# Performance work log

Hardware: AMD Instinct MI355X
Metric: run time of the kernel (lower is better)

## Reference

```python
import jax, jax.numpy as jnp
from jax import lax
import numpy as np

ALIGN = 6                 # AlignW: pad width up to a multiple of align_width=6
W_BITS = 5
A_BITS = 5
A_MASK = (1 << A_BITS) - 1  # direct_conv2d bit-packs activations: keep low A_bits
DN = ('NCHW', 'OIHW', 'NCHW')


def _align_w(a):
    pad = (-a.shape[-1]) % ALIGN
    if pad:
        a = jnp.pad(a, ((0, 0), (0, 0), (0, 0), (0, pad)))
    return a


def _conv_relu(a, w, b):
    # nn.Conv2d(kernel_size=3, padding=2) + ReLU
    y = lax.conv_general_dilated(a, w, (1, 1), [(2, 2), (2, 2)], dimension_numbers=DN)
    return jax.nn.relu(y + b[None, :, None, None])


def _dc_conv(a, w):
    # DC_layer: integer direct conv2d, W_bits-quantized weights, A_bits activations,
    # stride 1, no padding (valid).
    aq = jnp.bitwise_and(a, A_MASK)
    return lax.conv_general_dilated(aq, w, (1, 1), [(0, 0), (0, 0)], dimension_numbers=DN,
                                    preferred_element_type=jnp.int32)


def _maxpool2(a):
    if jnp.issubdtype(a.dtype, jnp.floating):
        init = np.float32(-np.inf)
    else:
        init = np.int32(np.iinfo(np.int32).min)
    return lax.reduce_window(a, init, lax.max, (1, 1, 2, 2), (1, 1, 2, 2), 'VALID')


def _forward(x, ws, bs, qs, fc_w, fc_b):
    a = x
    k = 0
    for n in (2, 2, 3):          # float VGG blocks: [64,64,M, 128,128,M, 256,256,256,M]
        for _ in range(n):
            a = _conv_relu(_align_w(a), ws[k], bs[k])
            k += 1
        a = _maxpool2(a)
    # dequant stub is identity; x.int() truncates toward zero (a >= 0 after ReLU)
    xi = lax.stop_gradient(a).astype(jnp.int32)
    k = 0
    for n in (3, 3):             # DC blocks: [512,512,512,M, 512,512,512,M]
        for _ in range(n):
            xi = _dc_conv(_align_w(xi), qs[k])
            k += 1
        xi = _maxpool2(xi)
    # classifier: AdaptiveAvgPool2d((1,1)) + Flatten + Linear(512, 1000)
    pooled = jnp.mean(xi.astype(jnp.float32), axis=(2, 3))
    return pooled @ fc_w.T + fc_b


def setup_inputs() -> dict:
    key = jax.random.key(0)
    ks = jax.random.split(key, 24)
    d = {}
    d['x'] = jax.random.uniform(ks[0], (16, 3, 224, 224), jnp.float32) * 8.0
    conv_cfg = [(3, 64), (64, 64), (64, 128), (128, 128), (128, 256), (256, 256), (256, 256)]
    for i, (ci, co) in enumerate(conv_cfg):
        d[f'w{i + 1}'] = jax.random.normal(ks[1 + i], (co, ci, 3, 3), jnp.float32) * 0.1
        d[f'b{i + 1}'] = jax.random.normal(ks[8 + i], (co,), jnp.float32) * 0.1
    dc_cfg = [(256, 512)] + [(512, 512)] * 5
    for i, (ci, co) in enumerate(dc_cfg):
        # torch.randint(0, 2**W_bits - 1, ...) -> values in [0, 2**W_bits - 2]
        d[f'q{i + 1}'] = jax.random.randint(ks[15 + i], (co, ci, 3, 3), 0, 2 ** W_BITS - 1, jnp.int32)
    d['fc_w'] = jax.random.normal(ks[21], (1000, 512), jnp.float32) * 0.02
    d['fc_b'] = jnp.zeros((1000,), jnp.float32)
    return d


def reference(x, w1, w2, w3, w4, w5, w6, w7,
              b1, b2, b3, b4, b5, b6, b7,
              q1, q2, q3, q4, q5, q6, fc_w, fc_b):
    ws = (w1, w2, w3, w4, w5, w6, w7)
    bs = (b1, b2, b3, b4, b5, b6, b7)
    qs = (q1, q2, q3, q4, q5, q6)
    return _forward(x, ws, bs, qs, fc_w, fc_b)
```

## Files before the change

### kernel.cpp

```cpp
#include <hip/hip_runtime.h>
#include <cstddef>


typedef float v2f __attribute__((ext_vector_type(2)));

static __device__ __forceinline__ int dot4(int a, int b, int c) {
#if __has_builtin(__builtin_amdgcn_sdot4)
    return __builtin_amdgcn_sdot4(a, b, c, false);
#else
    return c + (a & 255) * (b & 255)
             + ((a >> 8) & 255) * ((b >> 8) & 255)
             + ((a >> 16) & 255) * ((b >> 16) & 255)
             + ((a >> 24) & 255) * ((b >> 24) & 255);
#endif
}

static __device__ __forceinline__ void ld6f(const float* __restrict__ p, float v[6]) {
    const float4 a = *reinterpret_cast<const float4*>(p);
    const float2 b = *reinterpret_cast<const float2*>(p + 4);
    v[0] = a.x; v[1] = a.y; v[2] = a.z; v[3] = a.w; v[4] = b.x; v[5] = b.y;
}
static __device__ __forceinline__ void ld6i(const int* __restrict__ p, int v[6]) {
    const int4 a = *reinterpret_cast<const int4*>(p);
    const int2 b = *reinterpret_cast<const int2*>(p + 4);
    v[0] = a.x; v[1] = a.y; v[2] = a.z; v[3] = a.w; v[4] = b.x; v[5] = b.y;
}

static __device__ __forceinline__ void fmac8(const float v[3][6],
                                             const float* __restrict__ wr,
                                             v2f acc[8][2])
{
#pragma unroll
    for (int kh = 0; kh < 3; ++kh) {
        const v2f P0 = {v[kh][0], v[kh][1]};
        const v2f P1 = {v[kh][1], v[kh][2]};
        const v2f P2 = {v[kh][2], v[kh][3]};
        const v2f Q1 = {v[kh][3], v[kh][4]};
        const v2f Q2 = {v[kh][4], v[kh][5]};
#pragma unroll
        for (int c = 0; c < 8; ++c) {
            const float k0 = wr[c * 9 + kh * 3 + 0];
            const float k1 = wr[c * 9 + kh * 3 + 1];
            const float k2 = wr[c * 9 + kh * 3 + 2];
            const v2f k0p = {k0, k0}, k1p = {k1, k1}, k2p = {k2, k2};
            v2f a0 = acc[c][0];
            a0 = __builtin_elementwise_fma(P2, k2p, a0);
            a0 = __builtin_elementwise_fma(P1, k1p, a0);
            a0 = __builtin_elementwise_fma(P0, k0p, a0);
            acc[c][0] = a0;
            v2f a1 = acc[c][1];
            a1 = __builtin_elementwise_fma(Q2, k2p, a1);
            a1 = __builtin_elementwise_fma(Q1, k1p, a1);
            a1 = __builtin_elementwise_fma(P2, k0p, a1);
            acc[c][1] = a1;
        }
    }
}

static __device__ __forceinline__ void fmac4p(const float v[4][6],
                                              const float* __restrict__ wr,
                                              v2f acc[4][2][2])
{
#pragma unroll
    for (int r = 0; r < 2; ++r) {
#pragma unroll
        for (int kh = 0; kh < 3; ++kh) {
            const float* vv = v[r + kh];
            const v2f P0 = {vv[0], vv[1]};
            const v2f P1 = {vv[1], vv[2]};
            const v2f P2 = {vv[2], vv[3]};
            const v2f Q1 = {vv[3], vv[4]};
            const v2f Q2 = {vv[4], vv[5]};
#pragma unroll
            for (int c = 0; c < 4; ++c) {
                const float k0 = wr[c * 9 + kh * 3 + 0];
                const float k1 = wr[c * 9 + kh * 3 + 1];
                const float k2 = wr[c * 9 + kh * 3 + 2];
                const v2f k0p = {k0, k0}, k1p = {k1, k1}, k2p = {k2, k2};
                v2f a0 = acc[c][r][0];
                a0 = __builtin_elementwise_fma(P2, k2p, a0);
                a0 = __builtin_elementwise_fma(P1, k1p, a0);
                a0 = __builtin_elementwise_fma(P0, k0p, a0);
                acc[c][r][0] = a0;
                v2f a1 = acc[c][r][1];
                a1 = __builtin_elementwise_fma(Q2, k2p, a1);
                a1 = __builtin_elementwise_fma(Q1, k1p, a1);
                a1 = __builtin_elementwise_fma(P2, k0p, a1);
                acc[c][r][1] = a1;
            }
        }
    }
}

static __device__ __forceinline__ void dotc8(const int v[3][6],
                                             const int* __restrict__ wr,
                                             int acc[8][4])
{
#pragma unroll
    for (int kh = 0; kh < 3; ++kh) {
#pragma unroll
        for (int c = 0; c < 8; ++c) {
            const int k0 = wr[c * 9 + kh * 3 + 0];
            const int k1 = wr[c * 9 + kh * 3 + 1];
            const int k2 = wr[c * 9 + kh * 3 + 2];
#pragma unroll
            for (int t = 0; t < 4; ++t)
                acc[c][t] = dot4(v[kh][t], k0,
                            dot4(v[kh][t + 1], k1,
                            dot4(v[kh][t + 2], k2, acc[c][t])));
        }
    }
}

template<int CIN,int PH,int PW,int OH,int OW,int OPW,bool BORDER>
__global__ __launch_bounds__(256) void convf_k(
    const float* __restrict__ in, int instr,
    const float* __restrict__ wfp, const float* __restrict__ bias,
    float* __restrict__ out, int outstr, int total)
{
    constexpr int WB  = (OW + 3) / 4;
    constexpr int OPH = BORDER ? OH + 4 : OH;
    constexpr int OPL = OPH * OPW;
    const int s = blockIdx.z * 256 + threadIdx.x;
    if (s >= total) return;
    const int wb = s % WB;
    const int h  = (s / WB) % OH;
    const int n  = s / (WB * OH);
    const int w0 = wb * 4;
    const int cob = blockIdx.x;
    const int co0 = cob * 8;

    const float* ip = in + (size_t)n * instr + (size_t)h * PW + w0;
    const float* wl = wfp + (size_t)cob * CIN * 72;

    v2f acc[8][2];
#pragma unroll
    for (int c = 0; c < 8; ++c) { acc[c][0] = (v2f)0.f; acc[c][1] = (v2f)0.f; }

    float vb[3][6], vn[3][6];
#pragma unroll
    for (int kh = 0; kh < 3; ++kh) ld6f(ip + kh * PW, vb[kh]);

    if constexpr ((CIN & 1) == 0) {
        for (int ci = 0; ci < CIN; ci += 2) {
            ip += PH * PW;
#pragma unroll
            for (int kh = 0; kh < 3; ++kh) ld6f(ip + kh * PW, vn[kh]);
            fmac8(vb, wl + (size_t)ci * 72, acc);
            ip += PH * PW;
#pragma unroll
            for (int kh = 0; kh < 3; ++kh) ld6f(ip + kh * PW, vb[kh]);
            fmac8(vn, wl + (size_t)(ci + 1) * 72, acc);
        }
    } else {
        for (int ci = 0; ci < CIN; ++ci) {
            ip += PH * PW;
#pragma unroll
            for (int kh = 0; kh < 3; ++kh) ld6f(ip + kh * PW, vn[kh]);
            fmac8(vb, wl + (size_t)ci * 72, acc);
#pragma unroll
            for (int kh = 0; kh < 3; ++kh)
#pragma unroll
                for (int j = 0; j < 6; ++j) vb[kh][j] = vn[kh][j];
        }
    }

    float* ob = out + (size_t)n * outstr;
    const int ph  = BORDER ? h + 2 : h;
    const int pwo = BORDER ? 2 : 0;
#pragma unroll
    for (int c = 0; c < 8; ++c) {
        float* plane = ob + (size_t)(co0 + c) * OPL;
        float* row = plane + (size_t)ph * OPW;
        const float b = bias[co0 + c];
        float av[4] = {acc[c][0][0], acc[c][0][1], acc[c][1][0], acc[c][1][1]};
#pragma unroll
        for (int t = 0; t < 4; ++t)
            if (w0 + t < OW) { const float r = av[t] + b; row[pwo + w0 + t] = r > 0.f ? r : 0.f; }
        if (BORDER) {
            if (wb == 0) { row[0] = 0.f; row[1] = 0.f; }
            if (wb == WB - 1) { for (int pw = OW + 2; pw < OPW; ++pw) row[pw] = 0.f; }
            if (h == 0 || h == OH - 1) {
                float* r0 = plane + (h == 0 ? 0 : (size_t)(OH + 2) * OPW);
                for (int rr = 0; rr < 2; ++rr) {
                    float* br = r0 + (size_t)rr * OPW;
#pragma unroll
                    for (int t = 0; t < 4; ++t) if (w0 + t < OW) br[2 + w0 + t] = 0.f;
                    if (wb == 0) { br[0] = 0.f; br[1] = 0.f; }
                    if (wb == WB - 1) { for (int pw = OW + 2; pw < OPW; ++pw) br[pw] = 0.f; }
                }
            }
        }
    }
}

template<int CIN,int PH,int PW,int POH,int POW,int OPW,int OY,int OX,bool TOINT>
__global__ __launch_bounds__(256) void convfp_k(
    const float* __restrict__ in, int instr,
    const float* __restrict__ wfp, const float* __restrict__ bias,
    void* __restrict__ outv, int outstr, int total)
{
    constexpr int WBp = POW / 2;
    constexpr int OPH = POH + 2 * OY;
    constexpr int OPL = OPH * OPW;
    const int s = blockIdx.z * 256 + threadIdx.x;
    if (s >= total) return;
    const int pb = s % WBp;
    const int ph = (s / WBp) % POH;
    const int n  = s / (WBp * POH);
    const int cob = blockIdx.x;
    const int co0 = cob * 4;

    const float* ip = in + (size_t)n * instr + (size_t)(2 * ph) * PW + 4 * pb;
    const float* wl = wfp + (size_t)cob * CIN * 36;

    v2f acc[4][2][2];
#pragma unroll
    for (int c = 0; c < 4; ++c)
#pragma unroll
        for (int r = 0; r < 2; ++r) { acc[c][r][0] = (v2f)0.f; acc[c][r][1] = (v2f)0.f; }

    float vb[4][6], vn[4][6];
#pragma unroll
    for (int r = 0; r < 4; ++r) ld6f(ip + r * PW, vb[r]);

    for (int ci = 0; ci < CIN; ci += 2) {
        ip += PH * PW;
#pragma unroll
        for (int r = 0; r < 4; ++r) ld6f(ip + r * PW, vn[r]);
        fmac4p(vb, wl + (size_t)ci * 36, acc);
        ip += PH * PW;
#pragma unroll
        for (int r = 0; r < 4; ++r) ld6f(ip + r * PW, vb[r]);
        fmac4p(vn, wl + (size_t)(ci + 1) * 36, acc);
    }

#pragma unroll
    for (int c = 0; c < 4; ++c) {
        const float b = bias[co0 + c];
        float r00 = acc[c][0][0][0] + b; r00 = r00 > 0.f ? r00 : 0.f;
        float r01 = acc[c][0][0][1] + b; r01 = r01 > 0.f ? r01 : 0.f;
        float r02 = acc[c][0][1][0] + b; r02 = r02 > 0.f ? r02 : 0.f;
        float r03 = acc[c][0][1][1] + b; r03 = r03 > 0.f ? r03 : 0.f;
        float r10 = acc[c][1][0][0] + b; r10 = r10 > 0.f ? r10 : 0.f;
        float r11 = acc[c][1][0][1] + b; r11 = r11 > 0.f ? r11 : 0.f;
        float r12 = acc[c][1][1][0] + b; r12 = r12 > 0.f ? r12 : 0.f;
        float r13 = acc[c][1][1][1] + b; r13 = r13 > 0.f ? r13 : 0.f;
        float p0 = r00; p0 = p0 > r01 ? p0 : r01; p0 = p0 > r10 ? p0 : r10; p0 = p0 > r11 ? p0 : r11;
        float p1 = r02; p1 = p1 > r03 ? p1 : r03; p1 = p1 > r12 ? p1 : r12; p1 = p1 > r13 ? p1 : r13;

        if constexpr (TOINT) {
            int* plane = (int*)outv + (size_t)n * outstr + (size_t)(co0 + c) * OPL;
            int* row = plane + (size_t)(OY + ph) * OPW;
            row[OX + 2 * pb]     = (int)p0;
            row[OX + 2 * pb + 1] = (int)p1;
            if (pb == WBp - 1) { for (int pw = OX + POW; pw < OPW; ++pw) row[pw] = 0; }
        } else {
            float* plane = (float*)outv + (size_t)n * outstr + (size_t)(co0 + c) * OPL;
            float* row = plane + (size_t)(OY + ph) * OPW;
            row[OX + 2 * pb]     = p0;
            row[OX + 2 * pb + 1] = p1;
            if (OX > 0 && pb == 0) { row[0] = 0.f; row[1] = 0.f; }
            if (pb == WBp - 1) { for (int pw = OX + POW; pw < OPW; ++pw) row[pw] = 0.f; }
            if (OY > 0 && (ph == 0 || ph == POH - 1)) {
                float* r0 = plane + (ph == 0 ? 0 : (size_t)(OY + POH) * OPW);
                for (int rr = 0; rr < OY; ++rr) {
                    float* br = r0 + (size_t)rr * OPW;
                    br[OX + 2 * pb] = 0.f; br[OX + 2 * pb + 1] = 0.f;
                    if (pb == 0) { br[0] = 0.f; br[1] = 0.f; }
                    if (pb == WBp - 1) { for (int pw = OX + POW; pw < OPW; ++pw) br[pw] = 0.f; }
                }
            }
        }
    }
}

template<int CIN4,int PH,int PW,int OH,int OW,int OPW,bool PACKOUT>
__global__ __launch_bounds__(256) void convq_k(
    const int* __restrict__ in, int instr, const int* __restrict__ wqp,
    int* __restrict__ out, int outstr, int total)
{
    constexpr int WB  = (OW + 3) / 4;
    constexpr int OPL = OH * OPW;
    const int s = blockIdx.z * 256 + threadIdx.x;
    if (s >= total) return;
    const int wb = s % WB;
    const int h  = (s / WB) % OH;
    const int n  = s / (WB * OH);
    const int w0 = wb * 4;
    const int cob = blockIdx.x;
    const int co0 = cob * 8;

    const int* ip = in + (size_t)n * instr + (size_t)h * PW + w0;
    const int* wl = wqp + (size_t)cob * CIN4 * 72;

    int acc[8][4];
#pragma unroll
    for (int c = 0; c < 8; ++c)
#pragma unroll
        for (int t = 0; t < 4; ++t) acc[c][t] = 0;

    int vb[3][6], vn[3][6];
#pragma unroll
    for (int kh = 0; kh < 3; ++kh) ld6i(ip + kh * PW, vb[kh]);

    for (int ci = 0; ci < CIN4; ci += 2) {
        ip += PH * PW;
#pragma unroll
        for (int kh = 0; kh < 3; ++kh) ld6i(ip + kh * PW, vn[kh]);
        dotc8(vb, wl + (size_t)ci * 72, acc);
        ip += PH * PW;
#pragma unroll
        for (int kh = 0; kh < 3; ++kh) ld6i(ip + kh * PW, vb[kh]);
        dotc8(vn, wl + (size_t)(ci + 1) * 72, acc);
    }

    if (PACKOUT) {
        int* base = out + (size_t)n * outstr + (size_t)(cob * 2) * OPL + (size_t)h * OPW + w0;
#pragma unroll
        for (int t = 0; t < 4; ++t) {
            if (w0 + t < OW) {
                const int lo = (acc[0][t] & 31) | ((acc[1][t] & 31) << 8)
                             | ((acc[2][t] & 31) << 16) | ((acc[3][t] & 31) << 24);
                const int hi = (acc[4][t] & 31) | ((acc[5][t] & 31) << 8)
                             | ((acc[6][t] & 31) << 16) | ((acc[7][t] & 31) << 24);
                base[t] = lo;
                base[OPL + t] = hi;
            }
        }
        if (wb == WB - 1) {
            for (int pw = OW; pw < OPW; ++pw) { base[pw - w0] = 0; base[OPL + pw - w0] = 0; }
        }
    } else {
        int* ob = out + (size_t)n * outstr;
#pragma unroll
        for (int c = 0; c < 8; ++c) {
            int* row = ob + (size_t)(co0 + c) * OPL + (size_t)h * OPW;
#pragma unroll
            for (int t = 0; t < 4; ++t)
                if (w0 + t < OW) row[w0 + t] = acc[c][t];
            if (wb == WB - 1) { for (int pw = OW; pw < OPW; ++pw) row[pw] = 0; }
        }
    }
}

__global__ void pack_wf_k(const float* __restrict__ w, float* __restrict__ out,
                          int CIN, int TC, int total)
{
    const int i = blockIdx.x * 256 + threadIdx.x;
    if (i >= total) return;
    const int r = i % 9;
    const int c = (i / 9) % TC;
    const int t = i / (9 * TC);
    const int ci = t % CIN;
    const int cob = t / CIN;
    out[i] = w[(((size_t)cob * TC + c) * CIN + ci) * 9 + r];
}

__global__ void pack_wq_k(const int* __restrict__ q, int* __restrict__ out,
                          int CIN4, int total)
{
    const int i = blockIdx.x * 256 + threadIdx.x;
    if (i >= total) return;
    const int r = i % 9;
    const int c = (i / 9) % 8;
    const int t = i / 72;
    const int ci4 = t % CIN4;
    const int cob = t / CIN4;
    const int co = cob * 8 + c;
    const int* p = q + ((size_t)co * CIN4 * 4 + ci4 * 4) * 9 + r;
    out[i] = (p[0] & 255) | ((p[9] & 255) << 8) | ((p[18] & 255) << 16) | ((p[27] & 255) << 24);
}

template<int CIN,int PH,int PW>
__global__ void pack_a_k(const int* __restrict__ in, int instr,
                         int* __restrict__ out, int outstr, int total)
{
    const int i = blockIdx.x * 256 + threadIdx.x;
    if (i >= total) return;
    constexpr int CIN4 = CIN / 4;
    constexpr int PL = PH * PW;
    int t = i;
    const int pw = t % PW; t /= PW;
    const int ph = t % PH; t /= PH;
    const int c4 = t % CIN4; const int n = t / CIN4;
    const int* p = in + (size_t)n * instr + ((size_t)(c4 * 4) * PH + ph) * PW + pw;
    out[(size_t)n * outstr + ((size_t)c4 * PH + ph) * PW + pw] =
        (p[0] & 31) | ((p[PL] & 31) << 8) | ((p[2 * PL] & 31) << 16) | ((p[3 * PL] & 31) << 24);
}

template<int C,int HI,int WI,int HO,int WO,int OPH,int OPW>
__global__ void pool_i_k(const int* __restrict__ in, int instr,
                         int* __restrict__ out, int outstr, int total)
{
    const int i = blockIdx.x * 256 + threadIdx.x;
    if (i >= total) return;
    constexpr int OPL = OPH * OPW;
    int t = i;
    const int px = t % OPW; t /= OPW;
    const int py = t % OPH; t /= OPH;
    const int c  = t % C;   const int n = t / C;
    int v = 0;
    if (py < HO && px < WO) {
        const int* p = in + (size_t)n * instr + ((size_t)c * HI + 2 * py) * WI + 2 * px;
        int m = p[0];
        m = m > p[1] ? m : p[1];
        m = m > p[WI] ? m : p[WI];
        m = m > p[WI + 1] ? m : p[WI + 1];
        v = m;
    }
    out[(size_t)n * outstr + (size_t)c * OPL + (size_t)py * OPW + px] = v;
}

__global__ void copyin_k(const float* __restrict__ x, float* __restrict__ dst,
                         int outstr, int total)
{
    const int i = blockIdx.x * 256 + threadIdx.x;
    if (i >= total) return;
    int t = i;
    const int pw = t % 232; t /= 232;
    const int ph = t % 228; t /= 228;
    const int c  = t % 3;   const int n = t / 3;
    float v = 0.f;
    const int y = ph - 2, xx = pw - 2;
    if ((unsigned)y < 224u && (unsigned)xx < 224u)
        v = x[(size_t)n * 150528 + ((size_t)c * 224 + y) * 224 + xx];
    dst[(size_t)n * outstr + ((size_t)c * 228 + ph) * 232 + pw] = v;
}

__global__ void pool_mean_k(const int* __restrict__ in, int instr,
                            float* __restrict__ out, int outstr, int total)
{
    const int i = blockIdx.x * 256 + threadIdx.x;
    if (i >= total) return;
    const int n = i / 512, c = i % 512;
    const int* p = in + (size_t)n * instr + (size_t)c * 33;
    int s = 0;
#pragma unroll
    for (int j = 0; j < 33; ++j) s += p[j];
    out[(size_t)n * outstr + c] = (float)s / 33.0f;
}

__global__ void fc_k(const float* __restrict__ pooled, const float* __restrict__ w,
                     const float* __restrict__ b, float* __restrict__ out,
                     int nb, int n0)
{
    const int i = blockIdx.x * 256 + threadIdx.x;
    if (i >= nb * 1000) return;
    const int co = i % 1000;
    const int n  = i / 1000;
    const float* pv = pooled + (size_t)n * 512;
    const float* wr = w + (size_t)co * 512;
    float s = b[co];
    for (int c = 0; c < 512; ++c) s = fmaf(pv[c], wr[c], s);
    out[(size_t)(n0 + n) * 1000 + co] = s;
}

extern "C" void kernel_launch(void* const* d_in, const int* in_sizes, int n_in,
                              void* d_out, int out_size, void* d_ws, size_t ws_size,
                              hipStream_t stream)
{
    (void)n_in; (void)out_size;
    const float* x = (const float*)d_in[0];
    const float* W[7]; const float* Bv[7]; const int* Q[6];
    const bool inter = (in_sizes[2] == 64);
    for (int i = 0; i < 7; ++i) {
        if (inter) { W[i] = (const float*)d_in[1 + 2 * i]; Bv[i] = (const float*)d_in[2 + 2 * i]; }
        else       { W[i] = (const float*)d_in[1 + i];     Bv[i] = (const float*)d_in[8 + i];     }
    }
    for (int i = 0; i < 6; ++i) Q[i] = (const int*)d_in[15 + i];
    const float* fcw = (const float*)d_in[21];
    const float* fcb = (const float*)d_in[22];
    float* outp = (float*)d_out;

    static const int FCO[7]  = {64, 64, 128, 128, 256, 256, 256};
    static const int FCIN[7] = {3, 64, 64, 128, 128, 256, 256};
    static const int FTC[7]  = {8, 4, 8, 4, 8, 8, 4};
    static const int QCIN4[6] = {64, 128, 128, 128, 128, 128};
    size_t wfoff[7], wft = 0;
    for (int i = 0; i < 7; ++i) { wfoff[i] = wft; wft += (size_t)FCO[i] * FCIN[i] * 9; }
    size_t wqoff[6], wqt = 0;
    for (int i = 0; i < 6; ++i) { wqoff[i] = wqt; wqt += (size_t)512 * QCIN4[i] * 9 * 4; }
    const size_t WTOT = wft + wqt;

    float* wfb = (float*)d_ws;
    int*   wqb = (int*)((float*)d_ws + wft);
    for (int i = 0; i < 7; ++i) {
        const int total = FCO[i] * FCIN[i] * 9;
        pack_wf_k<<<(total + 255) / 256, 256, 0, stream>>>(W[i], wfb + wfoff[i], FCIN[i], FTC[i], total);
    }
    for (int i = 0; i < 6; ++i) {
        const int total = 512 * QCIN4[i] * 9;
        pack_wq_k<<<(total + 255) / 256, 256, 0, stream>>>(Q[i], wqb + wqoff[i], QCIN4[i], total);
    }

    const long long SZ_X0 = 158688,  SZ_F1 = 3532800, SZ_P1 = 936448;
    const long long SZ_F4 = 2027520, SZ_P2 = 580608,  SZ_F7 = 1264640;
    const long long SZ_F8 = 1440768, SZ_I0 = 360448,  SZ_PK1 = 90112;
    const long long SZ_D1 = 168960,  SZ_D2 = 157696,  SZ_D3 = 532480;
    const long long SZ_P4 = 159744,  SZ_PK4 = 39936,  SZ_D4 = 33792;
    const long long SZ_D5 = 27648,   SZ_D6 = 86016,   SZ_P5 = 16896;

    float* AR = (float*)d_ws + WTOT;
    long long AE2 = ((long long)(ws_size / 4) - (long long)WTOT - 20480) & ~3LL;

    int nbB = 16;
    for (;; nbB >>= 1) {
        if (nbB == 1) break;
        const long long f = nbB;
        const long long low = (nbB == 16) ? 0 : SZ_P1 * 16;
        const bool ok = (SZ_P1 * 16 + SZ_F4 * f <= AE2)
                     && (low + SZ_P2 * f <= AE2 - SZ_F4 * f)
                     && (low + SZ_F8 * f <= AE2 - SZ_F7 * f)
                     && (low + (SZ_PK1 + SZ_D1 + SZ_D2 + SZ_D3) * f <= AE2);
        if (ok) break;
    }
    int cA = 16;
    while (cA > 1 && SZ_P1 * 16 + (SZ_X0 + SZ_F1) * cA > AE2) cA >>= 1;

    const long long lowb = (nbB == 16) ? 0 : SZ_P1 * 16;
    float* tP1 = AR;
    float* tX0 = AR + SZ_P1 * 16;
    float* tF1 = tX0 + SZ_X0 * cA;
    float* tF4 = AR + (AE2 - SZ_F4 * nbB);
    float* tP2 = AR + lowb;
    float* tF7 = AR + (AE2 - SZ_F7 * nbB);
    float* tF8 = AR + lowb;
    int*   tI0 = (int*)(AR + (AE2 - SZ_I0 * nbB));
    int*   tPK1 = (int*)(AR + lowb);
    int*   tD1 = tPK1 + SZ_PK1 * nbB;
    int*   tD2 = tD1 + SZ_D1 * nbB;
    int*   tD3 = tD2 + SZ_D2 * nbB;
    int*   tP4 = (int*)(AR + lowb);
    int*   tPK4 = tP4 + SZ_P4 * nbB;
    int*   tD4 = tPK4 + SZ_PK4 * nbB;
    int*   tD5 = tD4 + SZ_D4 * nbB;
    int*   tD6 = tD5 + SZ_D5 * nbB;
    int*   tP5 = (int*)(AR + lowb);
    float* tPP = (float*)(tP5 + SZ_P5 * nbB);

    for (int a0 = 0; a0 < 16; a0 += cA) {
        const int nb = cA;
        {
            const int total = nb * 3 * 228 * 232;
            copyin_k<<<(total + 255) / 256, 256, 0, stream>>>(
                x + (size_t)a0 * 150528, tX0, (int)SZ_X0, total);
        }
        {
            const int total = nb * 226 * 58;
            dim3 g(8, 1, (total + 255) / 256);
            convf_k<3, 228, 232, 226, 230, 240, true><<<g, 256, 0, stream>>>(
                tX0, (int)SZ_X0, wfb + wfoff[0], Bv[0], tF1, (int)SZ_F1, total);
        }
        {
            const int total = nb * 114 * 59;
            dim3 g(16, 1, (total + 255) / 256);
            convfp_k<64, 230, 240, 114, 118, 124, 2, 2, false><<<g, 256, 0, stream>>>(
                tF1, (int)SZ_F1, wfb + wfoff[1], Bv[1],
                tP1 + (size_t)a0 * SZ_P1, (int)SZ_P1, total);
        }
    }

    for (int b0 = 0; b0 < 16; b0 += nbB) {
        const int nb = nbB;
        {
            const int total = nb * 116 * 31;
            dim3 g(16, 1, (total + 255) / 256);
            convf_k<64, 118, 124, 116, 122, 132, true><<<g, 256, 0, stream>>>(
                tP1 + (size_t)b0 * SZ_P1, (int)SZ_P1, wfb + wfoff[2], Bv[2],
                tF4, (int)SZ_F4, total);
        }
        {
            const int total = nb * 59 * 32;
            dim3 g(32, 1, (total + 255) / 256);
            convfp_k<128, 120, 132, 59, 64, 72, 2, 2, false><<<g, 256, 0, stream>>>(
                tF4, (int)SZ_F4, wfb + wfoff[3], Bv[3], tP2, (int)SZ_P2, total);
        }
        {
            const int total = nb * 61 * 17;
            dim3 g(32, 1, (total + 255) / 256);
            convf_k<128, 63, 72, 61, 68, 76, true><<<g, 256, 0, stream>>>(
                tP2, (int)SZ_P2, wfb + wfoff[4], Bv[4], tF7, (int)SZ_F7, total);
        }
        {
            const int total = nb * 63 * 19;
            dim3 g(32, 1, (total + 255) / 256);
            convf_k<256, 65, 76, 63, 74, 84, true><<<g, 256, 0, stream>>>(
                tF7, (int)SZ_F7, wfb + wfoff[5], Bv[5], tF8, (int)SZ_F8, total);
        }
        {
            const int total = nb * 32 * 20;
            dim3 g(64, 1, (total + 255) / 256);
            convfp_k<256, 67, 84, 32, 40, 44, 0, 0, true><<<g, 256, 0, stream>>>(
                tF8, (int)SZ_F8, wfb + wfoff[6], Bv[6], (void*)tI0, (int)SZ_I0, total);
        }
        {
            const int total = nb * 64 * 32 * 44;
            pack_a_k<256, 32, 44><<<(total + 255) / 256, 256, 0, stream>>>(
                tI0, (int)SZ_I0, tPK1, (int)SZ_PK1, total);
        }
        {
            const int total = nb * 30 * 10;
            dim3 g(64, 1, (total + 255) / 256);
            convq_k<64, 32, 44, 30, 40, 44, true><<<g, 256, 0, stream>>>(
                tPK1, (int)SZ_PK1, wqb + wqoff[0], tD1, (int)SZ_D1, total);
        }
        {
            const int total = nb * 28 * 10;
            dim3 g(64, 1, (total + 255) / 256);
            convq_k<128, 30, 44, 28, 40, 44, true><<<g, 256, 0, stream>>>(
                tD1, (int)SZ_D1, wqb + wqoff[1], tD2, (int)SZ_D2, total);
        }
        {
            const int total = nb * 26 * 10;
            dim3 g(64, 1, (total + 255) / 256);
            convq_k<128, 28, 44, 26, 40, 40, false><<<g, 256, 0, stream>>>(
                tD2, (int)SZ_D2, wqb + wqoff[2], tD3, (int)SZ_D3, total);
        }
        {
            const int total = nb * 512 * 13 * 24;
            pool_i_k<512, 26, 40, 13, 20, 13, 24><<<(total + 255) / 256, 256, 0, stream>>>(
                tD3, (int)SZ_D3, tP4, (int)SZ_P4, total);
        }
        {
            const int total = nb * 128 * 13 * 24;
            pack_a_k<512, 13, 24><<<(total + 255) / 256, 256, 0, stream>>>(
                tP4, (int)SZ_P4, tPK4, (int)SZ_PK4, total);
        }
        {
            const int total = nb * 11 * 6;
            dim3 g(64, 1, (total + 255) / 256);
            convq_k<128, 13, 24, 11, 22, 24, true><<<g, 256, 0, stream>>>(
                tPK4, (int)SZ_PK4, wqb + wqoff[3], tD4, (int)SZ_D4, total);
        }
        {
            const int total = nb * 9 * 6;
            dim3 g(64, 1, (total + 255) / 256);
            convq_k<128, 11, 24, 9, 22, 24, true><<<g, 256, 0, stream>>>(
                tD4, (int)SZ_D4, wqb + wqoff[4], tD5, (int)SZ_D5, total);
        }
        {
            const int total = nb * 7 * 6;
            dim3 g(64, 1, (total + 255) / 256);
            convq_k<128, 9, 24, 7, 22, 24, false><<<g, 256, 0, stream>>>(
                tD5, (int)SZ_D5, wqb + wqoff[5], tD6, (int)SZ_D6, total);
        }
        {
            const int total = nb * 512 * 33;
            pool_i_k<512, 7, 24, 3, 11, 3, 11><<<(total + 255) / 256, 256, 0, stream>>>(
                tD6, (int)SZ_D6, tP5, (int)SZ_P5, total);
        }
        {
            const int total = nb * 512;
            pool_mean_k<<<(total + 255) / 256, 256, 0, stream>>>(
                tP5, (int)SZ_P5, tPP, 512, total);
        }
        {
            const int total = nb * 1000;
            fc_k<<<(total + 255) / 256, 256, 0, stream>>>(tPP, fcw, fcb, outp, nb, b0);
        }
    }
}
```

Baseline: 5.998 ms.

## Compute two output rows per thread in conv kernels; fuse pack into conv/pool

The float and int8 direct-conv kernels now compute two output rows per thread and load four input rows, so each loaded input row and weight value serves more output work. The last float conv now writes bit-packed 5-bit activations directly, and the pool+pack kernels are fused into one poolpack kernel, which removes the intermediate int buffers and their launches. The FC kernel now reads float4 vectors, and the workspace layout is reorganised to match. The trade-off is higher register pressure from doubled accumulators and fewer threads per launch, which can reduce occupancy.

Result: slower. 6.468 ms (+7.8%).

```diff
diff --git a/kernel.cpp b/kernel.cpp
--- a/kernel.cpp
+++ b/kernel.cpp
@@ -26,33 +26,37 @@
     v[0] = a.x; v[1] = a.y; v[2] = a.z; v[3] = a.w; v[4] = b.x; v[5] = b.y;
 }
 
-static __device__ __forceinline__ void fmac8(const float v[3][6],
-                                             const float* __restrict__ wr,
-                                             v2f acc[8][2])
-{
-#pragma unroll
-    for (int kh = 0; kh < 3; ++kh) {
-        const v2f P0 = {v[kh][0], v[kh][1]};
-        const v2f P1 = {v[kh][1], v[kh][2]};
-        const v2f P2 = {v[kh][2], v[kh][3]};
-        const v2f Q1 = {v[kh][3], v[kh][4]};
-        const v2f Q2 = {v[kh][4], v[kh][5]};
-#pragma unroll
-        for (int c = 0; c < 8; ++c) {
-            const float k0 = wr[c * 9 + kh * 3 + 0];
-            const float k1 = wr[c * 9 + kh * 3 + 1];
-            const float k2 = wr[c * 9 + kh * 3 + 2];
-            const v2f k0p = {k0, k0}, k1p = {k1, k1}, k2p = {k2, k2};
-            v2f a0 = acc[c][0];
-            a0 = __builtin_elementwise_fma(P2, k2p, a0);
-            a0 = __builtin_elementwise_fma(P1, k1p, a0);
-            a0 = __builtin_elementwise_fma(P0, k0p, a0);
-            acc[c][0] = a0;
-            v2f a1 = acc[c][1];
-            a1 = __builtin_elementwise_fma(Q2, k2p, a1);
-            a1 = __builtin_elementwise_fma(Q1, k1p, a1);
-            a1 = __builtin_elementwise_fma(P2, k0p, a1);
-            acc[c][1] = a1;
+static __device__ __forceinline__ void fmac8r2(const float v[4][6],
+                                               const float* __restrict__ wr,
+                                               v2f acc[8][2][2])
+{
+#pragma unroll
+    for (int r = 0; r < 2; ++r) {
+#pragma unroll
+        for (int kh = 0; kh < 3; ++kh) {
+            const float* vv = v[r + kh];
+            const v2f P0 = {vv[0], vv[1]};
+            const v2f P1 = {vv[1], vv[2]};
+            const v2f P2 = {vv[2], vv[3]};
+            const v2f Q1 = {vv[3], vv[4]};
+            const v2f Q2 = {vv[4], vv[5]};
+#pragma unroll
+            for (int c = 0; c < 8; ++c) {
+                const float k0 = wr[c * 9 + kh * 3 + 0];
+                const float k1 = wr[c * 9 + kh * 3 + 1];
+                const float k2 = wr[c * 9 + kh * 3 + 2];
+                const v2f k0p = {k0, k0}, k1p = {k1, k1}, k2p = {k2, k2};
+                v2f a0 = acc[c][r][0];
+                a0 = __builtin_elementwise_fma(P2, k2p, a0);
+                a0 = __builtin_elementwise_fma(P1, k1p, a0);
+                a0 = __builtin_elementwise_fma(P0, k0p, a0);
+                acc[c][r][0] = a0;
+                v2f a1 = acc[c][r][1];
+                a1 = __builtin_elementwise_fma(Q2, k2p, a1);
+                a1 = __builtin_elementwise_fma(Q1, k1p, a1);
+                a1 = __builtin_elementwise_fma(P2, k0p, a1);
+                acc[c][r][1] = a1;
+            }
         }
     }
 }
@@ -92,24 +96,37 @@
     }
 }
 
-static __device__ __forceinline__ void dotc8(const int v[3][6],
-                                             const int* __restrict__ wr,
-                                             int acc[8][4])
-{
-#pragma unroll
-    for (int kh = 0; kh < 3; ++kh) {
-#pragma unroll
-        for (int c = 0; c < 8; ++c) {
-            const int k0 = wr[c * 9 + kh * 3 + 0];
-            const int k1 = wr[c * 9 + kh * 3 + 1];
-            const int k2 = wr[c * 9 + kh * 3 + 2];
-#pragma unroll
-            for (int t = 0; t < 4; ++t)
-                acc[c][t] = dot4(v[kh][t], k0,
-                            dot4(v[kh][t + 1], k1,
-                            dot4(v[kh][t + 2], k2, acc[c][t])));
-        }
-    }
+static __device__ __forceinline__ void dotc8r2(const int v[4][6],
+                                               const int* __restrict__ wr,
+                                               int acc[8][2][4])
+{
+#pragma unroll
+    for (int r = 0; r < 2; ++r) {
+#pragma unroll
+        for (int kh = 0; kh < 3; ++kh) {
+            const int* vv = v[r + kh];
+#pragma unroll
+            for (int c = 0; c < 8; ++c) {
+                const int k0 = wr[c * 9 + kh * 3 + 0];
+                const int k1 = wr[c * 9 + kh * 3 + 1];
+                const int k2 = wr[c * 9 + kh * 3 + 2];
+#pragma unroll
+                for (int t = 0; t < 4; ++t)
+                    acc[c][r][t] = dot4(vv[t], k0,
+                                   dot4(vv[t + 1], k1,
+                                   dot4(vv[t + 2], k2, acc[c][r][t])));
+            }
+        }
+    }
+}
+
+static __device__ __forceinline__ void zrow_border(float* br, int wb, int WB,
+                                                   int w0, int OW, int OPW)
+{
+#pragma unroll
+    for (int t = 0; t < 4; ++t) if (w0 + t < OW) br[2 + w0 + t] = 0.f;
+    if (wb == 0) { br[0] = 0.f; br[1] = 0.f; }
+    if (wb == WB - 1) { for (int pw = OW + 2; pw < OPW; ++pw) br[pw] = 0.f; }
 }
 
 template<int CIN,int PH,int PW,int OH,int OW,int OPW,bool BORDER>
@@ -119,82 +136,92 @@
     float* __restrict__ out, int outstr, int total)
 {
     constexpr int WB  = (OW + 3) / 4;
+    constexpr int HB  = (OH + 1) / 2;
     constexpr int OPH = BORDER ? OH + 4 : OH;
     constexpr int OPL = OPH * OPW;
     const int s = blockIdx.z * 256 + threadIdx.x;
     if (s >= total) return;
     const int wb = s % WB;
-    const int h  = (s / WB) % OH;
-    const int n  = s / (WB * OH);
+    const int hb = (s / WB) % HB;
+    const int n  = s / (WB * HB);
     const int w0 = wb * 4;
+    const int h0 = hb * 2;
+    const bool v1 = ((OH & 1) == 0) || (h0 + 1 < OH);
     const int cob = blockIdx.x;
     const int co0 = cob * 8;
 
-    const float* ip = in + (size_t)n * instr + (size_t)h * PW + w0;
+    const float* ip = in + (size_t)n * instr + (size_t)h0 * PW + w0;
     const float* wl = wfp + (size_t)cob * CIN * 72;
 
-    v2f acc[8][2];
-#pragma unroll
-    for (int c = 0; c < 8; ++c) { acc[c][0] = (v2f)0.f; acc[c][1] = (v2f)0.f; }
-
-    float vb[3][6], vn[3][6];
-#pragma unroll
-    for (int kh = 0; kh < 3; ++kh) ld6f(ip + kh * PW, vb[kh]);
+    v2f acc[8][2][2];
+#pragma unroll
+    for (int c = 0; c < 8; ++c)
+#pragma unroll
+        for (int r = 0; r < 2; ++r) { acc[c][r][0] = (v2f)0.f; acc[c][r][1] = (v2f)0.f; }
+
+    float vb[4][6], vn[4][6];
+#pragma unroll
+    for (int r = 0; r < 4; ++r) ld6f(ip + r * PW, vb[r]);
 
     if constexpr ((CIN & 1) == 0) {
         for (int ci = 0; ci < CIN; ci += 2) {
             ip += PH * PW;
 #pragma unroll
-            for (int kh = 0; kh < 3; ++kh) ld6f(ip + kh * PW, vn[kh]);
-            fmac8(vb, wl + (size_t)ci * 72, acc);
+            for (int r = 0; r < 4; ++r) ld6f(ip + r * PW, vn[r]);
+            fmac8r2(vb, wl + (size_t)ci * 72, acc);
             ip += PH * PW;
 #pragma unroll
-            for (int kh = 0; kh < 3; ++kh) ld6f(ip + kh * PW, vb[kh]);
-            fmac8(vn, wl + (size_t)(ci + 1) * 72, acc);
+            for (int r = 0; r < 4; ++r) ld6f(ip + r * PW, vb[r]);
+            fmac8r2(vn, wl + (size_t)(ci + 1) * 72, acc);
         }
     } else {
         for (int ci = 0; ci < CIN; ++ci) {
             ip += PH * PW;
 #pragma unroll
-            for (int kh = 0; kh < 3; ++kh) ld6f(ip + kh * PW, vn[kh]);
-            fmac8(vb, wl + (size_t)ci * 72, acc);
-#pragma unroll
-            for (int kh = 0; kh < 3; ++kh)
-#pragma unroll
-                for (int j = 0; j < 6; ++j) vb[kh][j] = vn[kh][j];
+            for (int r = 0; r < 4; ++r) ld6f(ip + r * PW, vn[r]);
+            fmac8r2(vb, wl + (size_t)ci * 72, acc);
+#pragma unroll
+            for (int r = 0; r < 4; ++r)
+#pragma unroll
+                for (int j = 0; j < 6; ++j) vb[r][j] = vn[r][j];
         }
     }
 
     float* ob = out + (size_t)n * outstr;
-    const int ph  = BORDER ? h + 2 : h;
-    const int pwo = BORDER ? 2 : 0;
 #pragma unroll
     for (int c = 0; c < 8; ++c) {
         float* plane = ob + (size_t)(co0 + c) * OPL;
-        float* row = plane + (size_t)ph * OPW;
         const float b = bias[co0 + c];
-        float av[4] = {acc[c][0][0], acc[c][0][1], acc[c][1][0], acc[c][1][1]};
-#pragma unroll
-        for (int t = 0; t < 4; ++t)
-            if (w0 + t < OW) { const float r = av[t] + b; row[pwo + w0 + t] = r > 0.f ? r : 0.f; }
+#pragma unroll
+        for (int r = 0; r < 2; ++r) {
+            if (r == 1 && !v1) break;
+            const int h = h0 + r;
+            float* row = plane + (size_t)(BORDER ? h + 2 : h) * OPW;
+            const float av[4] = {acc[c][r][0][0], acc[c][r][0][1],
+                                 acc[c][r][1][0], acc[c][r][1][1]};
+#pragma unroll
+            for (int t = 0; t < 4; ++t)
+                if (w0 + t < OW) { const float rr = av[t] + b;
+                    row[(BORDER ? 2 : 0) + w0 + t] = rr > 0.f ? rr : 0.f; }
+            if (BORDER) {
+                if (wb == 0) { row[0] = 0.f; row[1] = 0.f; }
+                if (wb == WB - 1) { for (int pw = OW + 2; pw < OPW; ++pw) row[pw] = 0.f; }
+            }
+        }
         if (BORDER) {
-            if (wb == 0) { row[0] = 0.f; row[1] = 0.f; }
-            if (wb == WB - 1) { for (int pw = OW + 2; pw < OPW; ++pw) row[pw] = 0.f; }
-            if (h == 0 || h == OH - 1) {
-                float* r0 = plane + (h == 0 ? 0 : (size_t)(OH + 2) * OPW);
-                for (int rr = 0; rr < 2; ++rr) {
-                    float* br = r0 + (size_t)rr * OPW;
-#pragma unroll
-                    for (int t = 0; t < 4; ++t) if (w0 + t < OW) br[2 + w0 + t] = 0.f;
-                    if (wb == 0) { br[0] = 0.f; br[1] = 0.f; }
-                    if (wb == WB - 1) { for (int pw = OW + 2; pw < OPW; ++pw) br[pw] = 0.f; }
-                }
-            }
-        }
-    }
-}
-
-template<int CIN,int PH,int PW,int POH,int POW,int OPW,int OY,int OX,bool TOINT>
+            if (h0 == 0) {
+                zrow_border(plane, wb, WB, w0, OW, OPW);
+                zrow_border(plane + OPW, wb, WB, w0, OW, OPW);
+            }
+            if (h0 == OH - 1 || h0 + 1 == OH - 1) {
+                zrow_border(plane + (size_t)(OH + 2) * OPW, wb, WB, w0, OW, OPW);
+                zrow_border(plane + (size_t)(OH + 3) * OPW, wb, WB, w0, OW, OPW);
+            }
+        }
+    }
+}
+
+template<int CIN,int PH,int PW,int POH,int POW,int OPW,int OY,int OX,int MODE>
 __global__ __launch_bounds__(256) void convfp_k(
     const float* __restrict__ in, int instr,
     const float* __restrict__ wfp, const float* __restrict__ bias,
@@ -235,6 +262,7 @@
         fmac4p(vn, wl + (size_t)(ci + 1) * 36, acc);
     }
 
+    float p[4][2];
 #pragma unroll
     for (int c = 0; c < 4; ++c) {
         const float b = bias[co0 + c];
@@ -248,18 +276,28 @@
         float r13 = acc[c][1][1][1] + b; r13 = r13 > 0.f ? r13 : 0.f;
         float p0 = r00; p0 = p0 > r01 ? p0 : r01; p0 = p0 > r10 ? p0 : r10; p0 = p0 > r11 ? p0 : r11;
         float p1 = r02; p1 = p1 > r03 ? p1 : r03; p1 = p1 > r12 ? p1 : r12; p1 = p1 > r13 ? p1 : r13;
-
-        if constexpr (TOINT) {
-            int* plane = (int*)outv + (size_t)n * outstr + (size_t)(co0 + c) * OPL;
-            int* row = plane + (size_t)(OY + ph) * OPW;
-            row[OX + 2 * pb]     = (int)p0;
-            row[OX + 2 * pb + 1] = (int)p1;
-            if (pb == WBp - 1) { for (int pw = OX + POW; pw < OPW; ++pw) row[pw] = 0; }
-        } else {
+        p[c][0] = p0; p[c][1] = p1;
+    }
+
+    if constexpr (MODE == 1) {
+        int* base = (int*)outv + (size_t)n * outstr + (size_t)cob * OPL
+                  + (size_t)(OY + ph) * OPW + OX + 2 * pb;
+        base[0] = (((int)p[0][0]) & 31) | ((((int)p[1][0]) & 31) << 8)
+                | ((((int)p[2][0]) & 31) << 16) | ((((int)p[3][0]) & 31) << 24);
+        base[1] = (((int)p[0][1]) & 31) | ((((int)p[1][1]) & 31) << 8)
+                | ((((int)p[2][1]) & 31) << 16) | ((((int)p[3][1]) & 31) << 24);
+        if (pb == WBp - 1) {
+            int* row = (int*)outv + (size_t)n * outstr + (size_t)cob * OPL
+                     + (size_t)(OY + ph) * OPW;
+            for (int pw = OX + POW; pw < OPW; ++pw) row[pw] = 0;
+        }
+    } else {
+#pragma unroll
+        for (int c = 0; c < 4; ++c) {
             float* plane = (float*)outv + (size_t)n * outstr + (size_t)(co0 + c) * OPL;
             float* row = plane + (size_t)(OY + ph) * OPW;
-            row[OX + 2 * pb]     = p0;
-            row[OX + 2 * pb + 1] = p1;
+            row[OX + 2 * pb]     = p[c][0];
+            row[OX + 2 * pb + 1] = p[c][1];
             if (OX > 0 && pb == 0) { row[0] = 0.f; row[1] = 0.f; }
             if (pb == WBp - 1) { for (int pw = OX + POW; pw < OPW; ++pw) row[pw] = 0.f; }
             if (OY > 0 && (ph == 0 || ph == POH - 1)) {
@@ -281,65 +319,79 @@
     int* __restrict__ out, int outstr, int total)
 {
     constexpr int WB  = (OW + 3) / 4;
+    constexpr int HB  = (OH + 1) / 2;
     constexpr int OPL = OH * OPW;
     const int s = blockIdx.z * 256 + threadIdx.x;
     if (s >= total) return;
     const int wb = s % WB;
-    const int h  = (s / WB) % OH;
-    const int n  = s / (WB * OH);
+    const int hb = (s / WB) % HB;
+    const int n  = s / (WB * HB);
     const int w0 = wb * 4;
+    const int h0 = hb * 2;
+    const bool v1 = ((OH & 1) == 0) || (h0 + 1 < OH);
     const int cob = blockIdx.x;
     const int co0 = cob * 8;
 
-    const int* ip = in + (size_t)n * instr + (size_t)h * PW + w0;
+    const int* ip = in + (size_t)n * instr + (size_t)h0 * PW + w0;
     const int* wl = wqp + (size_t)cob * CIN4 * 72;
 
-    int acc[8][4];
+    int acc[8][2][4];
 #pragma unroll
     for (int c = 0; c < 8; ++c)
 #pragma unroll
-        for (int t = 0; t < 4; ++t) acc[c][t] = 0;
-
-    int vb[3][6], vn[3][6];
-#pragma unroll
-    for (int kh = 0; kh < 3; ++kh) ld6i(ip + kh * PW, vb[kh]);
+        for (int r = 0; r < 2; ++r)
+#pragma unroll
+            for (int t = 0; t < 4; ++t) acc[c][r][t] = 0;
+
+    int vb[4][6], vn[4][6];
+#pragma unroll
+    for (int r = 0; r < 4; ++r) ld6i(ip + r * PW, vb[r]);
 
     for (int ci = 0; ci < CIN4; ci += 2) {
         ip += PH * PW;
 #pragma unroll
-        for (int kh = 0; kh < 3; ++kh) ld6i(ip + kh * PW, vn[kh]);
-        dotc8(vb, wl + (size_t)ci * 72, acc);
+        for (int r = 0; r < 4; ++r) ld6i(ip + r * PW, vn[r]);
+        dotc8r2(vb, wl + (size_t)ci * 72, acc);
         ip += PH * PW;
 #pragma unroll
-        for (int kh = 0; kh < 3; ++kh) ld6i(ip + kh * PW, vb[kh]);
-        dotc8(vn, wl + (size_t)(ci + 1) * 72, acc);
+        for (int r = 0; r < 4; ++r) ld6i(ip + r * PW, vb[r]);
+        dotc8r2(vn, wl + (size_t)(ci + 1) * 72, acc);
     }
 
     if (PACKOUT) {
-        int* base = out + (size_t)n * outstr + (size_t)(cob * 2) * OPL + (size_t)h * OPW + w0;
-#pragma unroll
-        for (int t = 0; t < 4; ++t) {
-            if (w0 + t < OW) {
-                const int lo = (acc[0][t] & 31) | ((acc[1][t] & 31) << 8)
-                             | ((acc[2][t] & 31) << 16) | ((acc[3][t] & 31) << 24);
-                const int hi = (acc[4][t] & 31) | ((acc[5][t] & 31) << 8)
-                             | ((acc[6][t] & 31) << 16) | ((acc[7][t] & 31) << 24);
-                base[t] = lo;
-                base[OPL + t] = hi;
-            }
-        }
-        if (wb == WB - 1) {
-            for (int pw = OW; pw < OPW; ++pw) { base[pw - w0] = 0; base[OPL + pw - w0] = 0; }
+#pragma unroll
+        for (int r = 0; r < 2; ++r) {
+            if (r == 1 && !v1) break;
+            int* base = out + (size_t)n * outstr + (size_t)(cob * 2) * OPL
+                      + (size_t)(h0 + r) * OPW + w0;
+#pragma unroll
+            for (int t = 0; t < 4; ++t) {
+                if (w0 + t < OW) {
+                    const int lo = (acc[0][r][t] & 31) | ((acc[1][r][t] & 31) << 8)
+                                 | ((acc[2][r][t] & 31) << 16) | ((acc[3][r][t] & 31) << 24);
+                    const int hi = (acc[4][r][t] & 31) | ((acc[5][r][t] & 31) << 8)
+                                 | ((acc[6][r][t] & 31) << 16) | ((acc[7][r][t] & 31) << 24);
+                    base[t] = lo;
+                    base[OPL + t] = hi;
+                }
+            }
+            if (wb == WB - 1) {
+                for (int pw = OW; pw < OPW; ++pw) { base[pw - w0] = 0; base[OPL + pw - w0] = 0; }
+            }
         }
     } else {
         int* ob = out + (size_t)n * outstr;
 #pragma unroll
         for (int c = 0; c < 8; ++c) {
-            int* row = ob + (size_t)(co0 + c) * OPL + (size_t)h * OPW;
-#pragma unroll
-            for (int t = 0; t < 4; ++t)
-                if (w0 + t < OW) row[w0 + t] = acc[c][t];
-            if (wb == WB - 1) { for (int pw = OW; pw < OPW; ++pw) row[pw] = 0; }
+#pragma unroll
+            for (int r = 0; r < 2; ++r) {
+                if (r == 1 && !v1) break;
+                int* row = ob + (size_t)(co0 + c) * OPL + (size_t)(h0 + r) * OPW;
+#pragma unroll
+                for (int t = 0; t < 4; ++t)
+                    if (w0 + t < OW) row[w0 + t] = acc[c][r][t];
+                if (wb == WB - 1) { for (int pw = OW; pw < OPW; ++pw) row[pw] = 0; }
+            }
         }
     }
 }
@@ -372,21 +424,30 @@
     out[i] = (p[0] & 255) | ((p[9] & 255) << 8) | ((p[18] & 255) << 16) | ((p[27] & 255) << 24);
 }
 
-template<int CIN,int PH,int PW>
-__global__ void pack_a_k(const int* __restrict__ in, int instr,
-                         int* __restrict__ out, int outstr, int total)
+template<int C4,int HI,int WI,int HO,int WO,int OPH,int OPW>
+__global__ void poolpack_k(const int* __restrict__ in, int instr,
+                           int* __restrict__ out, int outstr, int total)
 {
     const int i = blockIdx.x * 256 + threadIdx.x;
     if (i >= total) return;
-    constexpr int CIN4 = CIN / 4;
-    constexpr int PL = PH * PW;
     int t = i;
-    const int pw = t % PW; t /= PW;
-    const int ph = t % PH; t /= PH;
-    const int c4 = t % CIN4; const int n = t / CIN4;
-    const int* p = in + (size_t)n * instr + ((size_t)(c4 * 4) * PH + ph) * PW + pw;
-    out[(size_t)n * outstr + ((size_t)c4 * PH + ph) * PW + pw] =
-        (p[0] & 31) | ((p[PL] & 31) << 8) | ((p[2 * PL] & 31) << 16) | ((p[3 * PL] & 31) << 24);
+    const int px = t % OPW; t /= OPW;
+    const int py = t % OPH; t /= OPH;
+    const int c4 = t % C4;  const int n = t / C4;
+    int word = 0;
+    if (py < HO && px < WO) {
+#pragma unroll
+        for (int j = 0; j < 4; ++j) {
+            const int* p = in + (size_t)n * instr
+                         + ((size_t)(c4 * 4 + j) * HI + 2 * py) * WI + 2 * px;
+            int m = p[0];
+            m = m > p[1] ? m : p[1];
+            m = m > p[WI] ? m : p[WI];
+            m = m > p[WI + 1] ? m : p[WI + 1];
+            word |= (m & 31) << (8 * j);
+        }
+    }
+    out[(size_t)n * outstr + ((size_t)c4 * OPH + py) * OPW + px] = word;
 }
 
 template<int C,int HI,int WI,int HO,int WO,int OPH,int OPW>
@@ -449,10 +510,14 @@
     if (i >= nb * 1000) return;
     const int co = i % 1000;
     const int n  = i / 1000;
-    const float* pv = pooled + (size_t)n * 512;
-    const float* wr = w + (size_t)co * 512;
+    const float4* pv = (const float4*)(pooled + (size_t)n * 512);
+    const float4* wr = (const float4*)(w + (size_t)co * 512);
     float s = b[co];
-    for (int c = 0; c < 512; ++c) s = fmaf(pv[c], wr[c], s);
+    for (int c = 0; c < 128; ++c) {
+        const float4 a = pv[c], q = wr[c];
+        s = fmaf(a.x, q.x, s); s = fmaf(a.y, q.y, s);
+        s = fmaf(a.z, q.z, s); s = fmaf(a.w, q.w, s);
+    }
     out[(size_t)(n0 + n) * 1000 + co] = s;
 }
 
@@ -496,10 +561,11 @@
 
     const long long SZ_X0 = 158688,  SZ_F1 = 3532800, SZ_P1 = 936448;
     const long long SZ_F4 = 2027520, SZ_P2 = 580608,  SZ_F7 = 1264640;
-    const long long SZ_F8 = 1440768, SZ_I0 = 360448,  SZ_PK1 = 90112;
+    const long long SZ_F8 = 1440768, SZ_PK1 = 90112;
     const long long SZ_D1 = 168960,  SZ_D2 = 157696,  SZ_D3 = 532480;
-    const long long SZ_P4 = 159744,  SZ_PK4 = 39936,  SZ_D4 = 33792;
-    const long long SZ_D5 = 27648,   SZ_D6 = 86016,   SZ_P5 = 16896;
+    const long long SZ_PK4 = 39936,  SZ_D4 = 33792,   SZ_D5 = 27648;
+    const long long SZ_D6 = 86016,   SZ_P5 = 16896;
+    const long long DCH = SZ_D1 + SZ_D2 + SZ_D3 + SZ_PK4 + SZ_D4 + SZ_D5 + SZ_D6 + SZ_P5 + 512;
 
     float* AR = (float*)d_ws + WTOT;
     long long AE2 = ((long long)(ws_size / 4) - (long long)WTOT - 20480) & ~3LL;
@@ -512,7 +578,8 @@
         const bool ok = (SZ_P1 * 16 + SZ_F4 * f <= AE2)
                      && (low + SZ_P2 * f <= AE2 - SZ_F4 * f)
                      && (low + SZ_F8 * f <= AE2 - SZ_F7 * f)
-                     && (low + (SZ_PK1 + SZ_D1 + SZ_D2 + SZ_D3) * f <= AE2);
+                     && (low + SZ_F8 * f <= AE2 - SZ_PK1 * f)
+                     && (low + DCH * f <= AE2 - SZ_PK1 * f);
         if (ok) break;
     }
     int cA = 16;
@@ -526,17 +593,15 @@
     float* tP2 = AR + lowb;
     float* tF7 = AR + (AE2 - SZ_F7 * nbB);
     float* tF8 = AR + lowb;
-    int*   tI0 = (int*)(AR + (AE2 - SZ_I0 * nbB));
-    int*   tPK1 = (int*)(AR + lowb);
-    int*   tD1 = tPK1 + SZ_PK1 * nbB;
+    int*   tPK1 = (int*)(AR + (AE2 - SZ_PK1 * nbB));
+    int*   tD1 = (int*)(AR + lowb);
     int*   tD2 = tD1 + SZ_D1 * nbB;
     int*   tD3 = tD2 + SZ_D2 * nbB;
-    int*   tP4 = (int*)(AR + lowb);
-    int*   tPK4 = tP4 + SZ_P4 * nbB;
+    int*   tPK4 = tD3 + SZ_D3 * nbB;
     int*   tD4 = tPK4 + SZ_PK4 * nbB;
     int*   tD5 = tD4 + SZ_D4 * nbB;
     int*   tD6 = tD5 + SZ_D5 * nbB;
-    int*   tP5 = (int*)(AR + lowb);
+    int*   tP5 = tD6 + SZ_D6 * nbB;
     float* tPP = (float*)(tP5 + SZ_P5 * nbB);
 
     for (int a0 = 0; a0 < 16; a0 += cA) {
@@ -547,7 +612,7 @@
                 x + (size_t)a0 * 150528, tX0, (int)SZ_X0, total);
         }
         {
-            const int total = nb * 226 * 58;
+            const int total = nb * 113 * 58;
             dim3 g(8, 1, (total + 255) / 256);
             convf_k<3, 228, 232, 226, 230, 240, true><<<g, 256, 0, stream>>>(
                 tX0, (int)SZ_X0, wfb + wfoff[0], Bv[0], tF1, (int)SZ_F1, total);
@@ -555,7 +620,7 @@
         {
             const int total = nb * 114 * 59;
             dim3 g(16, 1, (total + 255) / 256);
-            convfp_k<64, 230, 240, 114, 118, 124, 2, 2, false><<<g, 256, 0, stream>>>(
+            convfp_k<64, 230, 240, 114, 118, 124, 2, 2, 0><<<g, 256, 0, stream>>>(
                 tF1, (int)SZ_F1, wfb + wfoff[1], Bv[1],
                 tP1 + (size_t)a0 * SZ_P1, (int)SZ_P1, total);
         }
@@ -564,7 +629,7 @@
     for (int b0 = 0; b0 < 16; b0 += nbB) {
         const int nb = nbB;
         {
-            const int total = nb * 116 * 31;
+            const int total = nb * 58 * 31;
             dim3 g(16, 1, (total + 255) / 256);
             convf_k<64, 118, 124, 116, 122, 132, true><<<g, 256, 0, stream>>>(
                 tP1 + (size_t)b0 * SZ_P1, (int)SZ_P1, wfb + wfoff[2], Bv[2],
@@ -573,17 +638,17 @@
         {
             const int total = nb * 59 * 32;
             dim3 g(32, 1, (total + 255) / 256);
-            convfp_k<128, 120, 132, 59, 64, 72, 2, 2, false><<<g, 256, 0, stream>>>(
+            convfp_k<128, 120, 132, 59, 64, 72, 2, 2, 0><<<g, 256, 0, stream>>>(
                 tF4, (int)SZ_F4, wfb + wfoff[3], Bv[3], tP2, (int)SZ_P2, total);
         }
         {
-            const int total = nb * 61 * 17;
+            const int total = nb * 31 * 17;
             dim3 g(32, 1, (total + 255) / 256);
             convf_k<128, 63, 72, 61, 68, 76, true><<<g, 256, 0, stream>>>(
                 tP2, (int)SZ_P2, wfb + wfoff[4], Bv[4], tF7, (int)SZ_F7, total);
         }
         {
-            const int total = nb * 63 * 19;
+            const int total = nb * 32 * 19;
             dim3 g(32, 1, (total + 255) / 256);
             convf_k<256, 65, 76, 63, 74, 84, true><<<g, 256, 0, stream>>>(
                 tF7, (int)SZ_F7, wfb + wfoff[5], Bv[5], tF8, (int)SZ_F8, total);
@@ -591,56 +656,46 @@
         {
             const int total = nb * 32 * 20;
             dim3 g(64, 1, (total + 255) / 256);
-            convfp_k<256, 67, 84, 32, 40, 44, 0, 0, true><<<g, 256, 0, stream>>>(
-                tF8, (int)SZ_F8, wfb + wfoff[6], Bv[6], (void*)tI0, (int)SZ_I0, total);
-        }
-        {
-            const int total = nb * 64 * 32 * 44;
-            pack_a_k<256, 32, 44><<<(total + 255) / 256, 256, 0, stream>>>(
-                tI0, (int)SZ_I0, tPK1, (int)SZ_PK1, total);
-        }
-        {
-            const int total = nb * 30 * 10;
+            convfp_k<256, 67, 84, 32, 40, 44, 0, 0, 1><<<g, 256, 0, stream>>>(
+                tF8, (int)SZ_F8, wfb + wfoff[6], Bv[6], (void*)tPK1, (int)SZ_PK1, total);
+        }
+        {
+            const int total = nb * 15 * 10;
             dim3 g(64, 1, (total + 255) / 256);
             convq_k<64, 32, 44, 30, 40, 44, true><<<g, 256, 0, stream>>>(
                 tPK1, (int)SZ_PK1, wqb + wqoff[0], tD1, (int)SZ_D1, total);
         }
         {
-            const int total = nb * 28 * 10;
+            const int total = nb * 14 * 10;
             dim3 g(64, 1, (total + 255) / 256);
             convq_k<128, 30, 44, 28, 40, 44, true><<<g, 256, 0, stream>>>(
                 tD1, (int)SZ_D1, wqb + wqoff[1], tD2, (int)SZ_D2, total);
         }
         {
-            const int total = nb * 26 * 10;
+            const int total = nb * 13 * 10;
             dim3 g(64, 1, (total + 255) / 256);
             convq_k<128, 28, 44, 26, 40, 40, false><<<g, 256, 0, stream>>>(
                 tD2, (int)SZ_D2, wqb + wqoff[2], tD3, (int)SZ_D3, total);
         }
         {
-            const int total = nb * 512 * 13 * 24;
-            pool_i_k<512, 26, 40, 13, 20, 13, 24><<<(total + 255) / 256, 256, 0, stream>>>(
-                tD3, (int)SZ_D3, tP4, (int)SZ_P4, total);
-        }
-        {
             const int total = nb * 128 * 13 * 24;
-            pack_a_k<512, 13, 24><<<(total + 255) / 256, 256, 0, stream>>>(
-                tP4, (int)SZ_P4, tPK4, (int)SZ_PK4, total);
-        }
-        {
-            const int total = nb * 11 * 6;
+            poolpack_k<128, 26, 40, 13, 20, 13, 24><<<(total + 255) / 256, 256, 0, stream>>>(
+                tD3, (int)SZ_D3, tPK4, (int)SZ_PK4, total);
+        }
+        {
+            const int total = nb * 6 * 6;
             dim3 g(64, 1, (total + 255) / 256);
             convq_k<128, 13, 24, 11, 22, 24, true><<<g, 256, 0, stream>>>(
                 tPK4, (int)SZ_PK4, wqb + wqoff[3], tD4, (int)SZ_D4, total);
         }
         {
-            const int total = nb * 9 * 6;
+            const int total = nb * 5 * 6;
             dim3 g(64, 1, (total + 255) / 256);
             convq_k<128, 11, 24, 9, 22, 24, true><<<g, 256, 0, stream>>>(
                 tD4, (int)SZ_D4, wqb + wqoff[4], tD5, (int)SZ_D5, total);
         }
         {
-            const int total = nb * 7 * 6;
+            const int total = nb * 4 * 6;
             dim3 g(64, 1, (total + 255) / 256);
             convq_k<128, 9, 24, 7, 22, 24, false><<<g, 256, 0, stream>>>(
                 tD5, (int)SZ_D5, wqb + wqoff[5], tD6, (int)SZ_D6, total);
```
